# Kernel optimization log

Measured on AMD Instinct MI355X. Metric: run time of the kernel, lower is better.

Reference implementation:

```python
import jax, jax.numpy as jnp
import numpy as np

B, N, ITERS = 8, 4096, 10  # batch, neurons (self.size), async-update sweeps


def setup_inputs() -> dict:
    key = jax.random.key(0)
    k1, k2, k3 = jax.random.split(key, 3)
    # bipolar {-1,+1} query patterns
    x = jnp.sign(jax.random.normal(k1, (B, N), dtype=jnp.float32))
    x = jnp.where(x == 0, 1.0, x)
    # symmetric Hebbian-style weight matrix with zero diagonal (as produced by fit())
    A = jax.random.normal(k2, (N, N), dtype=jnp.float32) / N
    W = 0.5 * (A + A.T)
    W = W - jnp.diag(jnp.diag(W))
    # one random neuron-visit permutation per (sample, sweep), replacing random.shuffle
    perm_keys = jax.random.split(k3, B * ITERS)
    perms = jax.vmap(lambda k: jax.random.permutation(k, N))(perm_keys)
    perms = perms.reshape(B, ITERS, N).astype(jnp.int32)
    return {"x": x, "weights": W, "perms": perms}


def reference(x, weights, perms):
    """Asynchronous Hopfield update: for each sample, sweep ITERS times over a
    random permutation of neurons, setting y[i] = sign(W[i] . y) sequentially."""
    flat_perms = perms.reshape(perms.shape[0], -1)  # [B, ITERS*N]

    def single(y0, perm_flat):
        def step(y, i):
            z = jnp.dot(weights[i], y)  # length-N dot, depends on previous updates
            return y.at[i].set(jnp.sign(z)), None
        y, _ = jax.lax.scan(step, y0, perm_flat)
        return y

    return jax.vmap(single)(x, flat_perms)  # [B, N]
```

## Files before the change

kernel.cpp:

```cpp
#include <hip/hip_runtime.h>

#define N 4096
#define B 8
#define ITERS 10
#define T (ITERS * N)
#define NT 256
#define E 16
#define WIN 1024
#define INFK 0xFFFFFFFFu
#define LIMIT 0x01000000u

__device__ __forceinline__ void lds_barrier() {
    asm volatile("s_waitcnt lgkmcnt(0)\n\ts_barrier" ::: "memory");
}

__global__ __launch_bounds__(256) void z0_gemv(const float* __restrict__ W,
                                               const float* __restrict__ x,
                                               double* __restrict__ Z0) {
    const int i0 = 2 * blockIdx.x;
    const int tid = threadIdx.x;
    const int lane = tid & 63;
    const int wid = tid >> 6;
    const float4* __restrict__ row0 = (const float4*)(W + (size_t)i0 * N);
    const float4* __restrict__ row1 = (const float4*)(W + (size_t)(i0 + 1) * N);
    const float4* __restrict__ xv = (const float4*)x;

    double acc0[B], acc1[B];
#pragma unroll
    for (int b = 0; b < B; ++b) { acc0[b] = 0.0; acc1[b] = 0.0; }

#pragma unroll
    for (int it = 0; it < 4; ++it) {
        const int c = tid + 256 * it;
        const float4 w0 = row0[c];
        const float4 w1 = row1[c];
#pragma unroll
        for (int b = 0; b < B; ++b) {
            const float4 xb = xv[b * (N / 4) + c];
            acc0[b] += (double)w0.x * (double)xb.x + (double)w0.y * (double)xb.y +
                       (double)w0.z * (double)xb.z + (double)w0.w * (double)xb.w;
            acc1[b] += (double)w1.x * (double)xb.x + (double)w1.y * (double)xb.y +
                       (double)w1.z * (double)xb.z + (double)w1.w * (double)xb.w;
        }
    }

#pragma unroll
    for (int off = 32; off > 0; off >>= 1) {
#pragma unroll
        for (int b = 0; b < B; ++b) {
            acc0[b] += __shfl_down(acc0[b], off, 64);
            acc1[b] += __shfl_down(acc1[b], off, 64);
        }
    }

    __shared__ double red[4][2][B];
    if (lane == 0) {
#pragma unroll
        for (int b = 0; b < B; ++b) { red[wid][0][b] = acc0[b]; red[wid][1][b] = acc1[b]; }
    }
    __syncthreads();
    if (tid < B) {
        Z0[(size_t)tid * N + i0] =
            red[0][0][tid] + red[1][0][tid] + red[2][0][tid] + red[3][0][tid];
        Z0[(size_t)tid * N + i0 + 1] =
            red[0][1][tid] + red[1][1][tid] + red[2][1][tid] + red[3][1][tid];
    }
}

__device__ __forceinline__ unsigned umin2(unsigned a, unsigned b) { return a < b ? a : b; }
__device__ __forceinline__ unsigned umin4(unsigned a, unsigned b, unsigned c, unsigned d) {
    return umin2(umin2(a, b), umin2(c, d));
}

template <int CTRL>
__device__ __forceinline__ unsigned dpp_min(unsigned v) {
    const int t = __builtin_amdgcn_update_dpp((int)v, (int)v, CTRL, 0xF, 0xF, false);
    return umin2(v, (unsigned)t);
}

__device__ __forceinline__ unsigned quarter_min(unsigned v) {
    v = dpp_min<0x111>(v);
    v = dpp_min<0x112>(v);
    v = dpp_min<0x114>(v);
    v = dpp_min<0x118>(v);
    return v;
}

__device__ __forceinline__ unsigned full_min(unsigned v) {
    v = quarter_min(v);
    v = dpp_min<0x142>(v);
    v = dpp_min<0x143>(v);
    return v;
}

__device__ __forceinline__ void fetch_row(const float* __restrict__ W, int i,
                                          int tid, float* wr) {
    const float4* __restrict__ rp = (const float4*)(W + (size_t)i * N) + 4 * tid;
    const float4 a = rp[0], c = rp[1], e = rp[2], f = rp[3];
    wr[0] = a.x;  wr[1] = a.y;  wr[2] = a.z;  wr[3] = a.w;
    wr[4] = c.x;  wr[5] = c.y;  wr[6] = c.z;  wr[7] = c.w;
    wr[8] = e.x;  wr[9] = e.y;  wr[10] = e.z; wr[11] = e.w;
    wr[12] = f.x; wr[13] = f.y; wr[14] = f.z; wr[15] = f.w;
}

#define FIXUP(ii)                                                         \
    do {                                                                  \
        if (tid == ((ii) >> 4)) {                                         \
            const int kk = (ii) & 15;                                     \
            _Pragma("unroll") for (int k = 0; k < E; ++k) if (k == kk) {  \
                ym[k] ^= 0x80000000u;                                     \
                sk[k] ^= 2u;                                              \
            }                                                             \
        }                                                                 \
    } while (0)

__global__ __launch_bounds__(256, 1) void hop_seq(const float* __restrict__ W,
                                                  const float* __restrict__ x,
                                                  const int* __restrict__ perms,
                                                  const double* __restrict__ Z0,
                                                  float* __restrict__ out) {
    const int b = blockIdx.x;
    const int tid = threadIdx.x;
    const int wid = tid >> 6;
    const int lane = tid & 63;

    __shared__ int wpos[N];
    __shared__ __align__(16) unsigned pubP[2][16];
    __shared__ __align__(16) unsigned pubV[2][4];

    double zj[E], zc[E];
    unsigned ym[E];
    unsigned sk[E];
    {
        const double* __restrict__ zsrc = Z0 + (size_t)b * N + E * tid;
#pragma unroll
        for (int k = 0; k < E; ++k) zj[k] = zsrc[k];
        const float4* __restrict__ xs = (const float4*)(x + (size_t)b * N);
#pragma unroll
        for (int q = 0; q < 4; ++q) {
            const float4 xv = xs[4 * tid + q];
            ym[4 * q + 0] = (xv.x > 0.f) ? 0xFFFFFFFFu : 0x7FFFFFFFu;
            ym[4 * q + 1] = (xv.y > 0.f) ? 0xFFFFFFFFu : 0x7FFFFFFFu;
            ym[4 * q + 2] = (xv.z > 0.f) ? 0xFFFFFFFFu : 0x7FFFFFFFu;
            ym[4 * q + 3] = (xv.w > 0.f) ? 0xFFFFFFFFu : 0x7FFFFFFFu;
        }
    }
    {
        const int4 z4 = make_int4(0, 0, 0, 0);
#pragma unroll
        for (int q = 0; q < 4; ++q) ((int4*)wpos)[tid + 256 * q] = z4;
    }
    lds_barrier();

    const int* __restrict__ perm_b = perms + (size_t)b * T;
    unsigned r = 0;

    for (int base = 0; base < T; base += WIN) {
        const int epoch = (base >> 10) + 1;
        const int4 iv = ((const int4*)(perm_b + base))[tid];
        wpos[iv.x] = (epoch << 10) | (4 * tid + 0);
        wpos[iv.y] = (epoch << 10) | (4 * tid + 1);
        wpos[iv.z] = (epoch << 10) | (4 * tid + 2);
        wpos[iv.w] = (epoch << 10) | (4 * tid + 3);
        lds_barrier();
#pragma unroll
        for (int q = 0; q < 4; ++q) {
            const int4 wp = ((const int4*)wpos)[4 * tid + q];
            const int e0 = 4 * q;
            const unsigned i0 = (unsigned)(E * tid + e0);
            sk[e0 + 0] = ((wp.x >> 10) == epoch)
                ? (((unsigned)(wp.x & 1023) << 14) | ((i0 + 0) << 2) | ((ym[e0 + 0] >> 30) & 2u)) : INFK;
            sk[e0 + 1] = ((wp.y >> 10) == epoch)
                ? (((unsigned)(wp.y & 1023) << 14) | ((i0 + 1) << 2) | ((ym[e0 + 1] >> 30) & 2u)) : INFK;
            sk[e0 + 2] = ((wp.z >> 10) == epoch)
                ? (((unsigned)(wp.z & 1023) << 14) | ((i0 + 2) << 2) | ((ym[e0 + 2] >> 30) & 2u)) : INFK;
            sk[e0 + 3] = ((wp.w >> 10) == epoch)
                ? (((unsigned)(wp.w & 1023) << 14) | ((i0 + 3) << 2) | ((ym[e0 + 3] >> 30) & 2u)) : INFK;
        }

        unsigned n = 0;
        unsigned wk1 = 0, wk2 = 0;
        unsigned ckR = 0;
        float w1[E], w2[E];

        for (;;) {
            unsigned ck1 = 0, ck2 = 0, ckP;
            int i1 = 0, i2 = 0;
            double d1 = 0.0, d2 = 0.0;
            if (n >= 1) {
                i1 = (int)((wk1 >> 2) & 4095u);
                d1 = (double)(-2 * ((int)(wk1 & 3u) - 1));
                ck1 = ((wk1 >> 14) + 1u) << 14;
                FIXUP(i1);
            }
            if (n == 2) {
                i2 = (int)((wk2 >> 2) & 4095u);
                d2 = (double)(-2 * ((int)(wk2 & 3u) - 1));
                ck2 = ((wk2 >> 14) + 1u) << 14;
                FIXUP(i2);
            }
            ckP = (n == 0) ? ckR : (n == 1) ? ck1 : ck2;

            unsigned key1 = INFK, keyP = INFK;
            if (n == 2) {
#pragma unroll
                for (int k = 0; k < E; ++k) {
                    const double a = fma(d1, (double)w1[k], zj[k]);
                    zc[k] = a;
                    const unsigned tm = ((unsigned)__double2hiint(a)) ^ ym[k];
                    key1 = umin2(key1, (sk[k] | (unsigned)(((int)tm) >> 31)) - ck1);
                    const double c = fma(d2, (double)w2[k], a);
                    zj[k] = c;
                    const unsigned tp = ((unsigned)__double2hiint(c)) ^ ym[k];
                    keyP = umin2(keyP, (sk[k] | (unsigned)(((int)tp) >> 31)) - ck2);
                }
            } else if (n == 1) {
#pragma unroll
                for (int k = 0; k < E; ++k) {
                    const double c = fma(d1, (double)w1[k], zj[k]);
                    zj[k] = c;
                    const unsigned tp = ((unsigned)__double2hiint(c)) ^ ym[k];
                    keyP = umin2(keyP, (sk[k] | (unsigned)(((int)tp) >> 31)) - ck1);
                }
            } else {
#pragma unroll
                for (int k = 0; k < E; ++k) {
                    const unsigned tp = ((unsigned)__double2hiint(zj[k])) ^ ym[k];
                    keyP = umin2(keyP, (sk[k] | (unsigned)(((int)tp) >> 31)) - ckR);
                }
            }

            const unsigned vP = quarter_min(keyP);
            const unsigned vV = full_min(key1);

            const unsigned p = r & 1u; ++r;
            if ((lane & 15) == 15) pubP[p][4 * wid + (lane >> 4)] = vP;
            if (lane == 63) pubV[p][wid] = vV;
            lds_barrier();

            const uint4 q0 = *(const uint4*)&pubP[p][0];
            const uint4 q1 = *(const uint4*)&pubP[p][4];
            const uint4 q2 = *(const uint4*)&pubP[p][8];
            const uint4 q3 = *(const uint4*)&pubP[p][12];
            const unsigned g1 = umin2(umin2(umin4(q0.x, q0.y, q0.z, q0.w),
                                            umin4(q1.x, q1.y, q1.z, q1.w)),
                                      umin2(umin4(q2.x, q2.y, q2.z, q2.w),
                                            umin4(q3.x, q3.y, q3.z, q3.w)));
            if (g1 < LIMIT)
                fetch_row(W, (int)(((g1 + ckP) >> 2) & 4095u), tid, w1);

            const unsigned a00 = (q0.x == g1) ? INFK : q0.x;
            const unsigned a01 = (q0.y == g1) ? INFK : q0.y;
            const unsigned a02 = (q0.z == g1) ? INFK : q0.z;
            const unsigned a03 = (q0.w == g1) ? INFK : q0.w;
            const unsigned a10 = (q1.x == g1) ? INFK : q1.x;
            const unsigned a11 = (q1.y == g1) ? INFK : q1.y;
            const unsigned a12 = (q1.z == g1) ? INFK : q1.z;
            const unsigned a13 = (q1.w == g1) ? INFK : q1.w;
            const unsigned a20 = (q2.x == g1) ? INFK : q2.x;
            const unsigned a21 = (q2.y == g1) ? INFK : q2.y;
            const unsigned a22 = (q2.z == g1) ? INFK : q2.z;
            const unsigned a23 = (q2.w == g1) ? INFK : q2.w;
            const unsigned a30 = (q3.x == g1) ? INFK : q3.x;
            const unsigned a31 = (q3.y == g1) ? INFK : q3.y;
            const unsigned a32 = (q3.z == g1) ? INFK : q3.z;
            const unsigned a33 = (q3.w == g1) ? INFK : q3.w;
            const unsigned g2 = umin2(umin2(umin4(a00, a01, a02, a03),
                                            umin4(a10, a11, a12, a13)),
                                      umin2(umin4(a20, a21, a22, a23),
                                            umin4(a30, a31, a32, a33)));

            if (n == 2) {
                const uint4 vv = *(const uint4*)&pubV[p][0];
                const unsigned gv = umin4(vv.x, vv.y, vv.z, vv.w);
                if (gv < ck2 - ck1) {
#pragma unroll
                    for (int k = 0; k < E; ++k) zj[k] = zc[k];
                    FIXUP(i2);
                    const unsigned vabs = gv + ck1;
                    if ((vabs >> 14) == (wk2 >> 14)) {
                        n = 0; ckR = ck2;
                    } else {
                        wk1 = vabs;
                        fetch_row(W, (int)((vabs >> 2) & 4095u), tid, w1);
                    }
                    continue;
                }
            }

            if (g1 >= LIMIT) break;
            wk1 = g1 + ckP; n = 1;
            if (g2 < LIMIT) {
                wk2 = g2 + ckP; n = 2;
                fetch_row(W, (int)((wk2 >> 2) & 4095u), tid, w2);
            }
        }
    }

    float4* __restrict__ os = (float4*)(out + (size_t)b * N);
#pragma unroll
    for (int q = 0; q < 4; ++q) {
        float4 o;
        o.x = (ym[4 * q + 0] & 0x80000000u) ? 1.0f : -1.0f;
        o.y = (ym[4 * q + 1] & 0x80000000u) ? 1.0f : -1.0f;
        o.z = (ym[4 * q + 2] & 0x80000000u) ? 1.0f : -1.0f;
        o.w = (ym[4 * q + 3] & 0x80000000u) ? 1.0f : -1.0f;
        os[4 * tid + q] = o;
    }
}

extern "C" void kernel_launch(void* const* d_in, const int* in_sizes, int n_in,
                              void* d_out, int out_size, void* d_ws, size_t ws_size,
                              hipStream_t stream) {
    const float* x = (const float*)d_in[0];
    const float* W = (const float*)d_in[1];
    const int* perms = (const int*)d_in[2];
    float* out = (float*)d_out;
    double* Z0 = (double*)d_ws;

    hipLaunchKernelGGL(z0_gemv, dim3(N / 2), dim3(256), 0, stream, W, x, Z0);
    hipLaunchKernelGGL(hop_seq, dim3(B), dim3(NT), 0, stream, W, x, perms, Z0, out);
}
```

Measured before the change: 2.216 ms.

## Prefetch third and fourth candidate rows and reuse them when selected

After picking the two lowest candidate neurons from the published per-quarter minima, the kernel also finds the third and fourth candidates and prefetches their weight rows into extra register buffers. A later row fetch reuses a prefetched buffer when the index matches, instead of loading the row from global memory on the critical serial path. The speculative validation branch now runs before the g1/g2 computation, and the first-row fetch is moved after the break check. The cost is 32 extra float registers per thread and wasted loads when the speculation is wrong. Stale cached indices are never invalidated, which is only safe because W is constant.

Result: slower. 2.775 ms (+25.2%).

```diff
diff --git a/kernel.cpp b/kernel.cpp
--- a/kernel.cpp
+++ b/kernel.cpp
@@ -93,6 +93,15 @@
     return v;
 }
 
+__device__ __forceinline__ unsigned min16(const unsigned* h) {
+    return umin2(umin2(umin4(h[0], h[1], h[2], h[3]), umin4(h[4], h[5], h[6], h[7])),
+                 umin2(umin4(h[8], h[9], h[10], h[11]), umin4(h[12], h[13], h[14], h[15])));
+}
+__device__ __forceinline__ void knock(unsigned* h, unsigned g) {
+#pragma unroll
+    for (int k = 0; k < 16; ++k) h[k] = (h[k] == g) ? INFK : h[k];
+}
+
 __device__ __forceinline__ void fetch_row(const float* __restrict__ W, int i,
                                           int tid, float* wr) {
     const float4* __restrict__ rp = (const float4*)(W + (size_t)i * N) + 4 * tid;
@@ -114,6 +123,18 @@
         }                                                                 \
     } while (0)
 
+#define GETROW(ii, dst)                                                     \
+    do {                                                                    \
+        const int _i = (ii);                                                \
+        if (_i == ci3) {                                                    \
+            _Pragma("unroll") for (int k = 0; k < E; ++k) dst[k] = pf3[k];  \
+        } else if (_i == ci4) {                                             \
+            _Pragma("unroll") for (int k = 0; k < E; ++k) dst[k] = pf4[k];  \
+        } else {                                                            \
+            fetch_row(W, _i, tid, dst);                                     \
+        }                                                                   \
+    } while (0)
+
 __global__ __launch_bounds__(256, 1) void hop_seq(const float* __restrict__ W,
                                                   const float* __restrict__ x,
                                                   const int* __restrict__ perms,
@@ -154,6 +175,9 @@
 
     const int* __restrict__ perm_b = perms + (size_t)b * T;
     unsigned r = 0;
+
+    float pf3[E], pf4[E];
+    int ci3 = -1, ci4 = -1;
 
     for (int base = 0; base < T; base += WIN) {
         const int epoch = (base >> 10) + 1;
@@ -238,61 +262,55 @@
             if (lane == 63) pubV[p][wid] = vV;
             lds_barrier();
 
+            const uint4 vv = *(const uint4*)&pubV[p][0];
             const uint4 q0 = *(const uint4*)&pubP[p][0];
             const uint4 q1 = *(const uint4*)&pubP[p][4];
             const uint4 q2 = *(const uint4*)&pubP[p][8];
             const uint4 q3 = *(const uint4*)&pubP[p][12];
-            const unsigned g1 = umin2(umin2(umin4(q0.x, q0.y, q0.z, q0.w),
-                                            umin4(q1.x, q1.y, q1.z, q1.w)),
-                                      umin2(umin4(q2.x, q2.y, q2.z, q2.w),
-                                            umin4(q3.x, q3.y, q3.z, q3.w)));
-            if (g1 < LIMIT)
-                fetch_row(W, (int)(((g1 + ckP) >> 2) & 4095u), tid, w1);
-
-            const unsigned a00 = (q0.x == g1) ? INFK : q0.x;
-            const unsigned a01 = (q0.y == g1) ? INFK : q0.y;
-            const unsigned a02 = (q0.z == g1) ? INFK : q0.z;
-            const unsigned a03 = (q0.w == g1) ? INFK : q0.w;
-            const unsigned a10 = (q1.x == g1) ? INFK : q1.x;
-            const unsigned a11 = (q1.y == g1) ? INFK : q1.y;
-            const unsigned a12 = (q1.z == g1) ? INFK : q1.z;
-            const unsigned a13 = (q1.w == g1) ? INFK : q1.w;
-            const unsigned a20 = (q2.x == g1) ? INFK : q2.x;
-            const unsigned a21 = (q2.y == g1) ? INFK : q2.y;
-            const unsigned a22 = (q2.z == g1) ? INFK : q2.z;
-            const unsigned a23 = (q2.w == g1) ? INFK : q2.w;
-            const unsigned a30 = (q3.x == g1) ? INFK : q3.x;
-            const unsigned a31 = (q3.y == g1) ? INFK : q3.y;
-            const unsigned a32 = (q3.z == g1) ? INFK : q3.z;
-            const unsigned a33 = (q3.w == g1) ? INFK : q3.w;
-            const unsigned g2 = umin2(umin2(umin4(a00, a01, a02, a03),
-                                            umin4(a10, a11, a12, a13)),
-                                      umin2(umin4(a20, a21, a22, a23),
-                                            umin4(a30, a31, a32, a33)));
-
             if (n == 2) {
-                const uint4 vv = *(const uint4*)&pubV[p][0];
                 const unsigned gv = umin4(vv.x, vv.y, vv.z, vv.w);
                 if (gv < ck2 - ck1) {
+                    const unsigned vabs = gv + ck1;
+                    const bool dem = ((vabs >> 14) == (wk2 >> 14));
+                    if (!dem) GETROW((int)((vabs >> 2) & 4095u), w1);
 #pragma unroll
                     for (int k = 0; k < E; ++k) zj[k] = zc[k];
                     FIXUP(i2);
-                    const unsigned vabs = gv + ck1;
-                    if ((vabs >> 14) == (wk2 >> 14)) {
+                    if (dem) {
                         n = 0; ckR = ck2;
                     } else {
                         wk1 = vabs;
-                        fetch_row(W, (int)((vabs >> 2) & 4095u), tid, w1);
                     }
                     continue;
                 }
             }
 
+            unsigned h[16];
+            h[0] = q0.x;  h[1] = q0.y;  h[2] = q0.z;  h[3] = q0.w;
+            h[4] = q1.x;  h[5] = q1.y;  h[6] = q1.z;  h[7] = q1.w;
+            h[8] = q2.x;  h[9] = q2.y;  h[10] = q2.z; h[11] = q2.w;
+            h[12] = q3.x; h[13] = q3.y; h[14] = q3.z; h[15] = q3.w;
+            const unsigned g1 = min16(h);
             if (g1 >= LIMIT) break;
             wk1 = g1 + ckP; n = 1;
+            GETROW((int)((wk1 >> 2) & 4095u), w1);
+            knock(h, g1);
+            const unsigned g2 = min16(h);
             if (g2 < LIMIT) {
                 wk2 = g2 + ckP; n = 2;
-                fetch_row(W, (int)((wk2 >> 2) & 4095u), tid, w2);
+                GETROW((int)((wk2 >> 2) & 4095u), w2);
+                knock(h, g2);
+                const unsigned g3 = min16(h);
+                if (g3 < LIMIT) {
+                    ci3 = (int)(((g3 + ckP) >> 2) & 4095u);
+                    fetch_row(W, ci3, tid, pf3);
+                    knock(h, g3);
+                    const unsigned g4 = min16(h);
+                    if (g4 < LIMIT) {
+                        ci4 = (int)(((g4 + ckP) >> 2) & 4095u);
+                        fetch_row(W, ci4, tid, pf4);
+                    }
+                }
             }
         }
     }
```
